# Kernel tuning notes

Measured on AMD Instinct MI355X. Metric: run time of the kernel, lower is better.

## Reference

```python
import jax, jax.numpy as jnp
import numpy as np

N, E = 25000, 100000
V_IN, V_OUT, E_IN, HID = 32, 64, 16, 128
H = 8
C = V_OUT // H  # per-head channels


def _glorot(key, shape, fan_in, fan_out):
    s = jnp.sqrt(6.0 / (fan_in + fan_out))
    return jax.random.uniform(key, shape, minval=-s, maxval=s, dtype=jnp.float32)


def setup_inputs() -> dict:
    key = jax.random.key(0)
    ks = jax.random.split(key, 8)
    x = jax.random.normal(ks[0], (N, V_IN), dtype=jnp.float32)
    e = jax.random.normal(ks[1], (E, E_IN), dtype=jnp.float32)
    e_idx = jax.random.randint(ks[2], (2, E), 0, N, dtype=jnp.int32)
    # edge MLP: Linear(E_IN, HID) -> ReLU -> Linear(HID, V_IN*V_OUT)
    W1 = _glorot(ks[3], (E_IN, HID), E_IN, HID)
    b1 = jnp.zeros((HID,), jnp.float32)
    W2 = _glorot(ks[4], (HID, V_IN * V_OUT), HID, V_IN * V_OUT)
    b2 = jnp.zeros((V_IN * V_OUT,), jnp.float32)
    att = _glorot(ks[5], (1, H, 2 * C), 2 * C, 2 * C)  # pyg glorot on [1,H,2C]
    bias = jnp.zeros((V_OUT,), jnp.float32)            # pyg zeros init
    root = _glorot(ks[6], (V_IN, V_OUT), V_IN, V_OUT)  # NNConv root weight
    return {"x": x, "e_idx": e_idx, "e": e, "W1": W1, "b1": b1,
            "W2": W2, "b2": b2, "att": att, "bias": bias, "root": root}


def reference(x, e_idx, e, W1, b1, W2, b2, att, bias, root):
    src, dst = e_idx[0], e_idx[1]  # source j -> target i (PyG flow)
    # per-edge weight matrices from edge MLP: [E, V_IN, V_OUT]
    w = (jax.nn.relu(e @ W1 + b1) @ W2 + b2).reshape(E, V_IN, V_OUT)
    # gather + per-edge matmul, split into heads: [E, H, C]
    xj = jnp.einsum('ei,eio->eo', x[src], w).reshape(E, H, C)
    xi = jnp.einsum('ei,eio->eo', x[dst], w).reshape(E, H, C)
    # attention logits: (cat([x_i, x_j], -1) * att).sum(-1) -> [E, H]
    alpha = (xi * att[:, :, :C]).sum(-1) + (xj * att[:, :, C:]).sum(-1)
    alpha = jax.nn.leaky_relu(alpha, negative_slope=0.2)
    # segment softmax over incoming edges of each target node
    m = jax.ops.segment_max(alpha, dst, num_segments=N)
    ea = jnp.exp(alpha - m[dst])
    s = jax.ops.segment_sum(ea, dst, num_segments=N)
    alpha = ea / (s[dst] + 1e-16)
    # message = attended x_j (+ per-edge bias as in source); dropout is eval no-op
    msg = (xj * alpha[..., None]).reshape(E, V_OUT) + bias
    out = jax.ops.segment_sum(msg, dst, num_segments=N)  # aggr='add'
    out = out + x @ root + bias  # NNConv root weight + forward bias
    return jax.nn.elu(out)  # wrapper: ELU; dropout no-op in eval
```

## Files before the change

kernel.cpp:

```cpp
#include <hip/hip_runtime.h>
#include <hip/hip_bf16.h>

#define N_NODES 25000
#define N_EDGES 100000
#define E_PAD   100032

typedef __attribute__((ext_vector_type(8))) short bf16x8;
typedef __attribute__((ext_vector_type(4))) float f32x4;

__device__ __forceinline__ unsigned short f2bf(float v) {
  __hip_bfloat16 hb = __float2bfloat16(v);
  return *reinterpret_cast<unsigned short*>(&hb);
}

__device__ __forceinline__ unsigned fkey(float f) {
  unsigned u = __float_as_uint(f);
  return (u & 0x80000000u) ? ~u : (u | 0x80000000u);
}
__device__ __forceinline__ float fdec(unsigned k) {
  return (k & 0x80000000u) ? __uint_as_float(k ^ 0x80000000u) : __uint_as_float(~k);
}

__global__ __launch_bounds__(256) void k_pre(const float* __restrict__ x,
    const float* __restrict__ root, const float* __restrict__ b2,
    const float* __restrict__ att, const float* __restrict__ bias,
    const float* __restrict__ W2, unsigned char* __restrict__ w2pk,
    float* __restrict__ out, float* __restrict__ xb,
    float* __restrict__ ab1, float* __restrict__ ab2,
    unsigned* __restrict__ mk, float* __restrict__ s_sum) {
  __shared__ float lxb[4][64];
  int b = blockIdx.x;
  if (b < 128) {
    int g = b * 256 + threadIdx.x;
    int lane = g & 63, s = (g >> 6) & 3, w = (g >> 8) & 3, i = g >> 10;
    int col = i * 64 + w * 16 + (lane & 15);
    int k0 = s * 32 + (lane >> 4) * 8;
    bf16x8 v;
    #pragma unroll
    for (int j = 0; j < 8; ++j)
      v[j] = (short)f2bf(W2[(size_t)(k0 + j) * 2048 + col]);
    *(bf16x8*)(w2pk + (size_t)g * 16) = v;
    return;
  }
  int g = (b - 128) * 256 + threadIdx.x;
  int n = g >> 6, o = g & 63;
  const float* xr = x + (size_t)n * 32;
  float ra = bias[o], xa = 0.f;
  #pragma unroll
  for (int i = 0; i < 32; ++i) {
    float xv = xr[i];
    ra += xv * root[i * 64 + o];
    xa += xv * b2[i * 64 + o];
  }
  out[g] = ra;
  xb[g] = xa;
  int ln = threadIdx.x >> 6;
  lxb[ln][o] = xa;
  __syncthreads();
  if (o < 8) {
    int hd = o;
    float s1 = 0.f, s2 = 0.f;
    #pragma unroll
    for (int c = 0; c < 8; ++c) {
      float v = lxb[ln][hd * 8 + c];
      s1 += v * att[hd * 16 + c];
      s2 += v * att[hd * 16 + 8 + c];
    }
    size_t idx = (size_t)n * 8 + hd;
    ab1[idx] = s1; ab2[idx] = s2; mk[idx] = 0u; s_sum[idx] = 0.f;
  }
}

__global__ __launch_bounds__(256)
__attribute__((amdgpu_waves_per_eu(2)))
void k_main(
    const float* __restrict__ x, const int* __restrict__ ei,
    const float* __restrict__ ef, const float* __restrict__ W1,
    const float* __restrict__ b1,
    const float* __restrict__ att, const float* __restrict__ ab1,
    const float* __restrict__ ab2,
    const unsigned char* __restrict__ w2pk,
    float* __restrict__ xj_out, float* __restrict__ alpha_out,
    unsigned* __restrict__ mk) {
  __shared__ unsigned char lds_h[16384];
  __shared__ float lds_xs[32 * 64];
  __shared__ float lds_xd[32 * 64];
  const int tid = threadIdx.x;
  const int lane = tid & 63;
  const int w = tid >> 6;
  const int e0 = blockIdx.x * 64;
  const int* srcp = ei;
  const int* dstp = ei + N_EDGES;

  {
    const int l15 = lane & 15;
    const int k0 = (lane >> 4) * 8;
    bf16x8 ha[4], hb[2];
    #pragma unroll
    for (int mt = 0; mt < 4; ++mt) {
      int e = e0 + mt * 16 + l15;
      if (e >= N_EDGES) e = N_EDGES - 1;
      bf16x8 v;
      if (k0 < 16) {
        const float* ap = ef + (size_t)e * 16 + k0;
        f32x4 a0 = *(const f32x4*)(ap);
        f32x4 a1 = *(const f32x4*)(ap + 4);
        #pragma unroll
        for (int t = 0; t < 4; ++t) {
          v[t]     = (short)f2bf(a0[t]);
          v[t + 4] = (short)f2bf(a1[t]);
        }
      } else {
        #pragma unroll
        for (int t = 0; t < 8; ++t) v[t] = 0;
      }
      ha[mt] = v;
    }
    #pragma unroll
    for (int nt = 0; nt < 2; ++nt) {
      int col = w * 32 + nt * 16 + l15;
      bf16x8 v;
      if (k0 < 16) {
        #pragma unroll
        for (int j = 0; j < 8; ++j)
          v[j] = (short)f2bf(W1[(k0 + j) * 128 + col]);
      } else {
        #pragma unroll
        for (int j = 0; j < 8; ++j) v[j] = 0;
      }
      hb[nt] = v;
    }
    const int lpb = (lane >> 4) * 4;
    const int byt = (lane & 7) * 2;
    #pragma unroll
    for (int nt = 0; nt < 2; ++nt) {
      float bv = b1[w * 32 + nt * 16 + l15];
      const int hi = (nt * 2 + (l15 >> 3)) << 4;
      #pragma unroll
      for (int mt = 0; mt < 4; ++mt) {
        f32x4 acc = {bv, bv, bv, bv};
        acc = __builtin_amdgcn_mfma_f32_16x16x32_bf16(ha[mt], hb[nt], acc, 0, 0, 0);
        unsigned base = (unsigned)(mt * 4 + w) * 1024u + (unsigned)hi * 16u + (unsigned)byt;
        #pragma unroll
        for (int r = 0; r < 4; ++r) {
          float hv = acc[r] > 0.f ? acc[r] : 0.f;
          *(unsigned short*)(lds_h + base + (lpb + r) * 16) = f2bf(hv);
        }
      }
    }
  }

  {
    int m = tid & 63;
    int half = (tid >> 6) & 1;
    int which = tid >> 7;
    int eIdx = e0 + m; if (eIdx >= N_EDGES) eIdx = N_EDGES - 1;
    int node = which ? dstp[eIdx] : srcp[eIdx];
    const f32x4* xr = (const f32x4*)(x + (size_t)node * 32 + half * 16);
    float* lx = which ? lds_xd : lds_xs;
    #pragma unroll
    for (int q = 0; q < 4; ++q) {
      f32x4 vv = xr[q];
      int i0 = half * 16 + q * 4;
      #pragma unroll
      for (int j = 0; j < 4; ++j) lx[(i0 + j) * 64 + m] = vv[j];
    }
  }
  __syncthreads();

  const unsigned char* bgp = w2pk + (size_t)w * 4096 + (size_t)lane * 16;
  f32x4 xj_acc[4] = {};
  f32x4 xi_acc[4] = {};
  const int rg4 = ((lane >> 4) & 3) * 4;
  const int lb16 = lane * 16;

  #pragma unroll 1
  for (int p = 0; p < 16; ++p) {
    const int i = 2 * p;
    bf16x8 bA[4], bB[4];
    #pragma unroll
    for (int s = 0; s < 4; ++s) {
      bA[s] = *(const bf16x8*)(bgp + (size_t)i * 16384 + s * 1024);
      bB[s] = *(const bf16x8*)(bgp + (size_t)(i + 1) * 16384 + s * 1024);
    }
    #pragma unroll
    for (int mt = 0; mt < 4; ++mt) {
      f32x4 gA = {0.f, 0.f, 0.f, 0.f};
      f32x4 gB = {0.f, 0.f, 0.f, 0.f};
      #pragma unroll
      for (int s = 0; s < 4; ++s) {
        bf16x8 a = *(const bf16x8*)(lds_h + (mt * 4 + s) * 1024 + lb16);
        gA = __builtin_amdgcn_mfma_f32_16x16x32_bf16(a, bA[s], gA, 0, 0, 0);
        gB = __builtin_amdgcn_mfma_f32_16x16x32_bf16(a, bB[s], gB, 0, 0, 0);
      }
      f32x4 xsv0 = *(const f32x4*)(lds_xs + i * 64 + mt * 16 + rg4);
      f32x4 xdv0 = *(const f32x4*)(lds_xd + i * 64 + mt * 16 + rg4);
      f32x4 xsv1 = *(const f32x4*)(lds_xs + (i + 1) * 64 + mt * 16 + rg4);
      f32x4 xdv1 = *(const f32x4*)(lds_xd + (i + 1) * 64 + mt * 16 + rg4);
      #pragma unroll
      for (int r = 0; r < 4; ++r) {
        xj_acc[mt][r] += xsv0[r] * gA[r] + xsv1[r] * gB[r];
        xi_acc[mt][r] += xdv0[r] * gA[r] + xdv1[r] * gB[r];
      }
    }
  }

  const int h2 = (lane >> 3) & 1;
  const int cc = lane & 7;
  const int head = 2 * w + h2;
  const float a1v = att[head * 16 + cc];
  const float a2v = att[head * 16 + 8 + cc];
  #pragma unroll
  for (int mt = 0; mt < 4; ++mt) {
    #pragma unroll
    for (int r = 0; r < 4; ++r) {
      int row = mt * 16 + rg4 + r;
      int eIdx = e0 + row;
      xj_out[(size_t)eIdx * 64 + w * 16 + (lane & 15)] = xj_acc[mt][r];
      float v = xi_acc[mt][r] * a1v + xj_acc[mt][r] * a2v;
      v += __shfl_xor(v, 1);
      v += __shfl_xor(v, 2);
      v += __shfl_xor(v, 4);
      if (cc == 0 && eIdx < N_EDGES) {
        int d = dstp[eIdx];
        float lg = v + ab1[(size_t)d * 8 + head] + ab2[(size_t)srcp[eIdx] * 8 + head];
        lg = lg > 0.f ? lg : 0.2f * lg;
        alpha_out[(size_t)eIdx * 8 + head] = lg;
        atomicMax(mk + (size_t)d * 8 + head, fkey(lg));
      }
    }
  }
}

__global__ __launch_bounds__(256) void k_exp(float* __restrict__ alpha,
    const int* __restrict__ ei, const unsigned* __restrict__ mk, float* __restrict__ s) {
  int g = blockIdx.x * 256 + threadIdx.x;
  int e = g >> 3, hd = g & 7;
  int d = ei[N_EDGES + e];
  float ea = expf(alpha[g] - fdec(mk[(size_t)d * 8 + hd]));
  alpha[g] = ea;
  atomicAdd(s + (size_t)d * 8 + hd, ea);
}

__global__ __launch_bounds__(256) void k_scatter(const float* __restrict__ xj,
    const float* __restrict__ xb, const float* __restrict__ alpha,
    const float* __restrict__ s, const int* __restrict__ ei,
    const float* __restrict__ bias, float* __restrict__ out) {
  int g = blockIdx.x * 256 + threadIdx.x;
  int e = g >> 6, o = g & 63, hd = o >> 3;
  int sidx = ei[e], d = ei[N_EDGES + e];
  float ea = alpha[(size_t)e * 8 + hd];
  float sv = s[(size_t)d * 8 + hd];
  float val = (xj[g] + xb[(size_t)sidx * 64 + o]) * (ea / (sv + 1e-16f)) + bias[o];
  atomicAdd(out + (size_t)d * 64 + o, val);
}

__global__ __launch_bounds__(256) void k_elu(float* __restrict__ out) {
  int g = blockIdx.x * 256 + threadIdx.x;
  float v = out[g];
  out[g] = v > 0.f ? v : expm1f(v);
}

extern "C" void kernel_launch(void* const* d_in, const int* in_sizes, int n_in,
                              void* d_out, int out_size, void* d_ws, size_t ws_size,
                              hipStream_t stream) {
  const float* x    = (const float*)d_in[0];
  const int*   eidx = (const int*)d_in[1];
  const float* ef   = (const float*)d_in[2];
  const float* W1   = (const float*)d_in[3];
  const float* b1   = (const float*)d_in[4];
  const float* W2   = (const float*)d_in[5];
  const float* b2   = (const float*)d_in[6];
  const float* att  = (const float*)d_in[7];
  const float* bias = (const float*)d_in[8];
  const float* root = (const float*)d_in[9];
  float* out = (float*)d_out;
  char* ws = (char*)d_ws;

  unsigned char* w2pk = (unsigned char*)(ws + 0);
  float* xb    = (float*)(ws + 524288);
  float* ab1   = (float*)(ws + 6924288);
  float* ab2   = (float*)(ws + 7724288);
  float* xj_ws = (float*)(ws + 8524288);
  float* al_ws = (float*)(ws + 34132480);
  unsigned* mk = (unsigned*)(ws + 37333504);
  float* s_sum = (float*)(ws + 38133504);

  k_pre  <<<128 + N_NODES * 64 / 256, 256, 0, stream>>>(x, root, b2, att, bias,
                                                  W2, w2pk, out, xb, ab1, ab2, mk, s_sum);
  k_main <<<E_PAD / 64, 256, 0, stream>>>(x, eidx, ef, W1, b1, att, ab1, ab2,
                                          w2pk, xj_ws, al_ws, mk);
  k_exp  <<<N_EDGES * 8 / 256, 256, 0, stream>>>(al_ws, eidx, mk, s_sum);
  k_scatter<<<N_EDGES * 64 / 256, 256, 0, stream>>>(xj_ws, xb, al_ws, s_sum, eidx, bias, out);
  k_elu  <<<N_NODES * 64 / 256, 256, 0, stream>>>(out);
}
```

Measured before the change: 155.3 us.

## Retile k_main MFMA work as 2x2 edge/column warp grid with register-resident A fragments

Each warp now owns half the edges (32 rows) and half the output columns (32 cols) instead of all 64 edges for 16 columns. The hidden-activation A fragments for the warp's edges are loaded from LDS once into registers and pinned there, rather than reloaded from LDS every iteration. This removes repeated LDS reads of A, but each warp now streams twice as many W2 fragments per i from global or cache. The loop runs over all 32 i without pairing, and register pressure rises from the held A fragments.

```diff
diff --git a/kernel.cpp b/kernel.cpp
--- a/kernel.cpp
+++ b/kernel.cpp
@@ -32,8 +32,8 @@
   int b = blockIdx.x;
   if (b < 128) {
     int g = b * 256 + threadIdx.x;
-    int lane = g & 63, s = (g >> 6) & 3, w = (g >> 8) & 3, i = g >> 10;
-    int col = i * 64 + w * 16 + (lane & 15);
+    int lane = g & 63, s = (g >> 6) & 3, cg = (g >> 8) & 3, i = g >> 10;
+    int col = i * 64 + cg * 16 + (lane & 15);
     int k0 = s * 32 + (lane >> 4) * 8;
     bf16x8 v;
     #pragma unroll
@@ -88,6 +88,8 @@
   const int tid = threadIdx.x;
   const int lane = tid & 63;
   const int w = tid >> 6;
+  const int eh = w >> 1;
+  const int ch = w & 1;
   const int e0 = blockIdx.x * 64;
   const int* srcp = ei;
   const int* dstp = ei + N_EDGES;
@@ -168,65 +170,78 @@
   }
   __syncthreads();
 
-  const unsigned char* bgp = w2pk + (size_t)w * 4096 + (size_t)lane * 16;
-  f32x4 xj_acc[4] = {};
-  f32x4 xi_acc[4] = {};
+  const int lb16 = lane * 16;
+  bf16x8 af[2][4];
+  #pragma unroll
+  for (int mt2 = 0; mt2 < 2; ++mt2)
+    #pragma unroll
+    for (int s = 0; s < 4; ++s)
+      af[mt2][s] = *(const bf16x8*)(lds_h + ((eh * 2 + mt2) * 4 + s) * 1024 + lb16);
+  #pragma unroll
+  for (int mt2 = 0; mt2 < 2; ++mt2)
+    #pragma unroll
+    for (int s = 0; s < 4; ++s)
+      asm volatile("" : "+v"(af[mt2][s]));
+
+  const unsigned char* bgp = w2pk + (size_t)(ch * 2) * 4096 + (size_t)lane * 16;
+  f32x4 xj_acc[2][2] = {};
+  f32x4 xi_acc[2][2] = {};
   const int rg4 = ((lane >> 4) & 3) * 4;
-  const int lb16 = lane * 16;
 
   #pragma unroll 1
-  for (int p = 0; p < 16; ++p) {
-    const int i = 2 * p;
-    bf16x8 bA[4], bB[4];
-    #pragma unroll
-    for (int s = 0; s < 4; ++s) {
-      bA[s] = *(const bf16x8*)(bgp + (size_t)i * 16384 + s * 1024);
-      bB[s] = *(const bf16x8*)(bgp + (size_t)(i + 1) * 16384 + s * 1024);
-    }
-    #pragma unroll
-    for (int mt = 0; mt < 4; ++mt) {
-      f32x4 gA = {0.f, 0.f, 0.f, 0.f};
-      f32x4 gB = {0.f, 0.f, 0.f, 0.f};
-      #pragma unroll
-      for (int s = 0; s < 4; ++s) {
-        bf16x8 a = *(const bf16x8*)(lds_h + (mt * 4 + s) * 1024 + lb16);
-        gA = __builtin_amdgcn_mfma_f32_16x16x32_bf16(a, bA[s], gA, 0, 0, 0);
-        gB = __builtin_amdgcn_mfma_f32_16x16x32_bf16(a, bB[s], gB, 0, 0, 0);
-      }
-      f32x4 xsv0 = *(const f32x4*)(lds_xs + i * 64 + mt * 16 + rg4);
-      f32x4 xdv0 = *(const f32x4*)(lds_xd + i * 64 + mt * 16 + rg4);
-      f32x4 xsv1 = *(const f32x4*)(lds_xs + (i + 1) * 64 + mt * 16 + rg4);
-      f32x4 xdv1 = *(const f32x4*)(lds_xd + (i + 1) * 64 + mt * 16 + rg4);
-      #pragma unroll
-      for (int r = 0; r < 4; ++r) {
-        xj_acc[mt][r] += xsv0[r] * gA[r] + xsv1[r] * gB[r];
-        xi_acc[mt][r] += xdv0[r] * gA[r] + xdv1[r] * gB[r];
-      }
-    }
-  }
-
+  for (int i = 0; i < 32; ++i) {
+    bf16x8 bf[2][4];
+    #pragma unroll
+    for (int nt = 0; nt < 2; ++nt)
+      #pragma unroll
+      for (int s = 0; s < 4; ++s)
+        bf[nt][s] = *(const bf16x8*)(bgp + (size_t)i * 16384 + nt * 4096 + s * 1024);
+    #pragma unroll
+    for (int mt2 = 0; mt2 < 2; ++mt2) {
+      f32x4 xsv = *(const f32x4*)(lds_xs + i * 64 + (eh * 2 + mt2) * 16 + rg4);
+      f32x4 xdv = *(const f32x4*)(lds_xd + i * 64 + (eh * 2 + mt2) * 16 + rg4);
+      #pragma unroll
+      for (int nt = 0; nt < 2; ++nt) {
+        f32x4 g = {0.f, 0.f, 0.f, 0.f};
+        #pragma unroll
+        for (int s = 0; s < 4; ++s)
+          g = __builtin_amdgcn_mfma_f32_16x16x32_bf16(af[mt2][s], bf[nt][s], g, 0, 0, 0);
+        #pragma unroll
+        for (int r = 0; r < 4; ++r) {
+          xj_acc[mt2][nt][r] += xsv[r] * g[r];
+          xi_acc[mt2][nt][r] += xdv[r] * g[r];
+        }
+      }
+    }
+  }
+
+  const int l15 = lane & 15;
   const int h2 = (lane >> 3) & 1;
   const int cc = lane & 7;
-  const int head = 2 * w + h2;
-  const float a1v = att[head * 16 + cc];
-  const float a2v = att[head * 16 + 8 + cc];
   #pragma unroll
-  for (int mt = 0; mt < 4; ++mt) {
-    #pragma unroll
-    for (int r = 0; r < 4; ++r) {
-      int row = mt * 16 + rg4 + r;
-      int eIdx = e0 + row;
-      xj_out[(size_t)eIdx * 64 + w * 16 + (lane & 15)] = xj_acc[mt][r];
-      float v = xi_acc[mt][r] * a1v + xj_acc[mt][r] * a2v;
-      v += __shfl_xor(v, 1);
-      v += __shfl_xor(v, 2);
-      v += __shfl_xor(v, 4);
-      if (cc == 0 && eIdx < N_EDGES) {
-        int d = dstp[eIdx];
-        float lg = v + ab1[(size_t)d * 8 + head] + ab2[(size_t)srcp[eIdx] * 8 + head];
-        lg = lg > 0.f ? lg : 0.2f * lg;
-        alpha_out[(size_t)eIdx * 8 + head] = lg;
-        atomicMax(mk + (size_t)d * 8 + head, fkey(lg));
+  for (int mt2 = 0; mt2 < 2; ++mt2) {
+    #pragma unroll
+    for (int nt = 0; nt < 2; ++nt) {
+      int head = ch * 4 + nt * 2 + h2;
+      float a1v = att[head * 16 + cc];
+      float a2v = att[head * 16 + 8 + cc];
+      #pragma unroll
+      for (int r = 0; r < 4; ++r) {
+        int row = eh * 32 + mt2 * 16 + rg4 + r;
+        int eIdx = e0 + row;
+        int o = ch * 32 + nt * 16 + l15;
+        xj_out[(size_t)eIdx * 64 + o] = xj_acc[mt2][nt][r];
+        float v = xi_acc[mt2][nt][r] * a1v + xj_acc[mt2][nt][r] * a2v;
+        v += __shfl_xor(v, 1);
+        v += __shfl_xor(v, 2);
+        v += __shfl_xor(v, 4);
+        if (cc == 0 && eIdx < N_EDGES) {
+          int d = dstp[eIdx];
+          float lg = v + ab1[(size_t)d * 8 + head] + ab2[(size_t)srcp[eIdx] * 8 + head];
+          lg = lg > 0.f ? lg : 0.2f * lg;
+          alpha_out[(size_t)eIdx * 8 + head] = lg;
+          atomicMax(mk + (size_t)d * 8 + head, fkey(lg));
+        }
       }
     }
   }
```

After: 169.6 us. +9.2%, slower.
